# Kernel tuning notes

Measured on AMD Instinct MI355X. Metric: run time of the kernel, lower is better.

The kernel has to match this reference:

```python
import jax, jax.numpy as jnp
import numpy as np

B, S, D, H = 4, 2048, 1024, 16
HD = D // H  # head_dim = 64


def setup_inputs() -> dict:
    key = jax.random.key(0)
    ks = jax.random.split(key, 6)
    scale = 0.02
    x = jax.random.normal(ks[0], (B, S, D), dtype=jnp.float32)
    # per-head projection weights, torch Linear is y = x @ W.T; store as [H, D, HD]
    Wq = jax.random.normal(ks[1], (H, D, HD), dtype=jnp.float32) * scale
    Wk = jax.random.normal(ks[2], (H, D, HD), dtype=jnp.float32) * scale
    Wv = jax.random.normal(ks[3], (H, D, HD), dtype=jnp.float32) * scale
    Wo = jax.random.normal(ks[4], (D, D), dtype=jnp.float32) * scale  # torch [out, in]
    bo = jax.random.normal(ks[5], (D,), dtype=jnp.float32) * scale
    return {"x": x, "Wq": Wq, "Wk": Wk, "Wv": Wv, "Wo": Wo, "bo": bo}


def reference(x, Wq, Wk, Wv, Wo, bo):
    # project: [B,S,D] x [H,D,HD] -> [B,H,S,HD]
    q = jnp.einsum("bsd,hde->bhse", x, Wq)
    k = jnp.einsum("bsd,hde->bhse", x, Wk)
    v = jnp.einsum("bsd,hde->bhse", x, Wv)
    scores = jnp.einsum("bhse,bhte->bhst", q, k) / jnp.sqrt(jnp.float32(HD))
    causal = jnp.tril(jnp.ones((S, S), dtype=bool))  # same as registered tril mask
    scores = jnp.where(causal, scores, -jnp.inf)
    w = jax.nn.softmax(scores, axis=-1)
    out = jnp.einsum("bhst,bhte->bhse", w, v)  # [B,H,S,HD]
    # concat heads along feature dim: [B,S,H*HD] = [B,S,D]
    out = out.transpose(0, 2, 1, 3).reshape(B, S, D)
    # output projection: torch Linear y = x @ W.T + b
    return jnp.einsum("bsd,od->bso", out, Wo) + bo
```

## Files before the change

kernel.cpp:

```cpp
#include <hip/hip_runtime.h>
#include <hip/hip_bf16.h>

typedef __bf16 bf16x8 __attribute__((ext_vector_type(8)));
typedef float f32x4 __attribute__((ext_vector_type(4)));
typedef unsigned short u16x4 __attribute__((ext_vector_type(4)));
typedef unsigned short u16x8 __attribute__((ext_vector_type(8)));
typedef unsigned uint4v __attribute__((ext_vector_type(4)));

#define B_ 4
#define S_ 2048
#define D_ 1024
#define H_ 16
#define HD_ 64

__device__ __forceinline__ unsigned short f2bf(float f) {
  unsigned u = __float_as_uint(f);
  u += 0x7fff + ((u >> 16) & 1);
  return (unsigned short)(u >> 16);
}

__device__ __forceinline__ void gload16(const void* g, void* l) {
  __builtin_amdgcn_global_load_lds((const __attribute__((address_space(1))) unsigned int*)g,
                                   (__attribute__((address_space(3))) unsigned int*)l,
                                   16, 0, 0);
}

__global__ void pack_x_k(const float* __restrict__ in, unsigned short* __restrict__ out, int n4) {
  int i = blockIdx.x * blockDim.x + threadIdx.x;
  int stride = gridDim.x * blockDim.x;
  for (; i < n4; i += stride) {
    float4 v = reinterpret_cast<const float4*>(in)[i];
    u16x4 o = {f2bf(v.x), f2bf(v.y), f2bf(v.z), f2bf(v.w)};
    reinterpret_cast<u16x4*>(out)[i] = o;
  }
}

__global__ void pack_wqkv_k(const float* __restrict__ Wq, const float* __restrict__ Wk,
                            const float* __restrict__ Wv, unsigned short* __restrict__ Wt) {
  int o = blockIdx.x * blockDim.x + threadIdx.x;
  int n = o >> 10;
  int d = o & 1023;
  const float* W = (n < 1024) ? Wq : (n < 2048) ? Wk : Wv;
  int nn = n & 1023;
  int h = nn >> 6, e = nn & 63;
  Wt[o] = f2bf(W[(h << 16) + (d << 6) + e]);
}

__global__ __launch_bounds__(512, 2) void gemm256_k(const unsigned short* __restrict__ A,
                                                    const unsigned short* __restrict__ Bt,
                                                    unsigned short* __restrict__ C,
                                                    int M, int N, int K) {
  __shared__ __align__(16) unsigned short lds[2][2][2][128 * 64];
  const int tid = threadIdx.x;
  const int wid = tid >> 6, lane = tid & 63;
  const int r = lane & 15, g = lane >> 4;
  const int wm = wid >> 2, wn = wid & 3;

  int id = blockIdx.y * gridDim.x + blockIdx.x;
  const int cpx = (gridDim.x * gridDim.y) >> 3;
  id = (id & 7) * cpx + (id >> 3);
  const long arow0 = (long)(id % gridDim.x) * 256;
  const long bcol0 = (long)(id / gridDim.x) * 256;

  const f32x4 z4 = {0.f, 0.f, 0.f, 0.f};
  f32x4 acc[8][4];
#pragma unroll
  for (int m = 0; m < 8; ++m)
#pragma unroll
    for (int n = 0; n < 4; ++n) acc[m][n] = z4;

  auto stage_half = [&](int kt, int op, int h) {
    const unsigned short* src = op ? Bt + (bcol0 + 128 * h) * K : A + (arow0 + 128 * h) * K;
    const int k0 = kt << 6;
    unsigned short* base = &lds[kt & 1][op][h][0];
#pragma unroll
    for (int c = 0; c < 2; ++c) {
      const int j = c * 512 + (wid << 6) + lane;
      const int row = j >> 3, cc = j & 7;
      const int ccs = cc ^ (row & 7);
      gload16(src + (long)row * K + k0 + ccs * 8, base + (c * 512 + (wid << 6)) * 8);
    }
  };

  const int nk = K >> 6;
  stage_half(0, 0, 0);
  stage_half(0, 1, 0);
  stage_half(0, 0, 1);
  stage_half(0, 1, 1);
  stage_half(1, 0, 0);
  stage_half(1, 1, 0);
  asm volatile("s_waitcnt vmcnt(8)" ::: "memory");
  asm volatile("s_barrier" ::: "memory");

  for (int t = 0; t < nk; ++t) {
    const int buf = t & 1;
#pragma unroll
    for (int ph = 0; ph < 4; ++ph) {
      const int mh = ph >> 1, nh = ph & 1;
      bf16x8 af[4][2], bfv[2][2];
#pragma unroll
      for (int i = 0; i < 4; ++i)
#pragma unroll
        for (int kk = 0; kk < 2; ++kk) {
          const int rowh = (2 * i + wm) * 16 + r;
          af[i][kk] = *(const bf16x8*)&lds[buf][0][mh][rowh * 64 + (((kk << 2) + g) ^ (rowh & 7)) * 8];
        }
#pragma unroll
      for (int j = 0; j < 2; ++j)
#pragma unroll
        for (int kk = 0; kk < 2; ++kk) {
          const int rowh = (4 * j + wn) * 16 + r;
          bfv[j][kk] = *(const bf16x8*)&lds[buf][1][nh][rowh * 64 + (((kk << 2) + g) ^ (rowh & 7)) * 8];
        }
      if (ph == 0) { if (t + 1 < nk) stage_half(t + 1, 0, 1); }
      if (ph == 1) { if (t + 1 < nk) stage_half(t + 1, 1, 1); }
      if (ph == 2) { if (t + 2 < nk) stage_half(t + 2, 0, 0); }
      if (ph == 3) { if (t + 2 < nk) stage_half(t + 2, 1, 0); }
      asm volatile("s_barrier" ::: "memory");
      __builtin_amdgcn_s_setprio(1);
#pragma unroll
      for (int kk = 0; kk < 2; ++kk)
#pragma unroll
        for (int i = 0; i < 4; ++i)
#pragma unroll
          for (int j = 0; j < 2; ++j)
            acc[4 * mh + i][2 * nh + j] = __builtin_amdgcn_mfma_f32_16x16x32_bf16(
                af[i][kk], bfv[j][kk], acc[4 * mh + i][2 * nh + j], 0, 0, 0);
      __builtin_amdgcn_s_setprio(0);
      if (ph == 0) {
        if (t + 1 < nk) asm volatile("s_waitcnt vmcnt(6)" ::: "memory");
        else            asm volatile("s_waitcnt vmcnt(0)" ::: "memory");
      }
      if (ph == 3) {
        if (t + 2 < nk)      asm volatile("s_waitcnt vmcnt(8)" ::: "memory");
        else if (t + 1 < nk) asm volatile("s_waitcnt vmcnt(4)" ::: "memory");
      }
      asm volatile("s_waitcnt lgkmcnt(0)\n\ts_barrier" ::: "memory");
    }
  }

#pragma unroll
  for (int m = 0; m < 8; ++m)
#pragma unroll
    for (int n = 0; n < 4; ++n)
#pragma unroll
      for (int rr = 0; rr < 4; ++rr) {
        const long row = arow0 + (2 * m + wm) * 16 + g * 4 + rr;
        const long col = bcol0 + (4 * n + wn) * 16 + r;
        C[row * N + col] = f2bf(acc[m][n][rr]);
      }
}

__global__ __launch_bounds__(256, 2) void gemm_bt_k(const unsigned short* __restrict__ A,
                                                    const unsigned short* __restrict__ Bt,
                                                    float* __restrict__ C,
                                                    const float* __restrict__ bias,
                                                    int M, int N, int K) {
  __shared__ __align__(16) unsigned short lA[2][128 * 64];
  __shared__ __align__(16) unsigned short lB[2][128 * 64];
  const int tid = threadIdx.x;
  const int wid = tid >> 6, lane = tid & 63;
  const int r = lane & 15, g = lane >> 4;
  const long arow0 = (long)blockIdx.x * 128;
  const long brow0 = (long)blockIdx.y * 128;
  const int wr = (wid >> 1) * 64, wc = (wid & 1) * 64;

  const f32x4 z4 = {0.f, 0.f, 0.f, 0.f};
  f32x4 acc[4][4];
#pragma unroll
  for (int m = 0; m < 4; ++m)
#pragma unroll
    for (int n = 0; n < 4; ++n) acc[m][n] = z4;

  auto stage = [&](int buf, int k0) {
#pragma unroll
    for (int c = 0; c < 4; ++c) {
      const int j = c * 256 + wid * 64 + lane;
      const int row = j >> 3, col = (j & 7) * 8;
      gload16(A + (arow0 + row) * K + k0 + col, &lA[buf][(c * 256 + wid * 64) * 8]);
      gload16(Bt + (brow0 + row) * K + k0 + col, &lB[buf][(c * 256 + wid * 64) * 8]);
    }
  };

  stage(0, 0);
  __syncthreads();
  const int nk = K >> 6;
  for (int kt = 0; kt < nk; ++kt) {
    const int cur = kt & 1;
    if (kt + 1 < nk) stage(cur ^ 1, (kt + 1) << 6);
#pragma unroll
    for (int kk = 0; kk < 2; ++kk) {
      bf16x8 af[4], bfr[4];
#pragma unroll
      for (int m = 0; m < 4; ++m)
        af[m] = *(const bf16x8*)&lA[cur][(wr + m * 16 + r) * 64 + kk * 32 + g * 8];
#pragma unroll
      for (int n = 0; n < 4; ++n)
        bfr[n] = *(const bf16x8*)&lB[cur][(wc + n * 16 + r) * 64 + kk * 32 + g * 8];
#pragma unroll
      for (int m = 0; m < 4; ++m)
#pragma unroll
        for (int n = 0; n < 4; ++n)
          acc[m][n] = __builtin_amdgcn_mfma_f32_16x16x32_bf16(af[m], bfr[n], acc[m][n], 0, 0, 0);
    }
    __syncthreads();
  }

#pragma unroll
  for (int m = 0; m < 4; ++m) {
#pragma unroll
    for (int n = 0; n < 4; ++n) {
#pragma unroll
      for (int rr = 0; rr < 4; ++rr) {
        const long row = arow0 + wr + m * 16 + g * 4 + rr;
        const long col = brow0 + wc + n * 16 + r;
        C[row * N + col] = acc[m][n][rr] + bias[col];
      }
    }
  }
}

__global__ __launch_bounds__(256, 2) void attn_k(const unsigned short* __restrict__ qkv,
                                                 unsigned short* __restrict__ out) {
  __shared__ __align__(16) unsigned short lK[2][64 * 64];
  __shared__ __align__(16) unsigned short lVt[2][64 * 64];

  const int tid = threadIdx.x, wid = tid >> 6, lane = tid & 63;
  const int r = lane & 15, g = lane >> 4;
  const int bh = blockIdx.x;
  const int b = bh >> 4, h = bh & 15;
  const int qb = 15 - (int)blockIdx.y;
  const int q0 = qb * 128;

  const long base = ((long)b * S_) * 3072 + h * 64;
  const unsigned short* Qg = qkv + base;
  const unsigned short* Kg = qkv + base + 1024;
  const unsigned short* Vg = qkv + base + 2048;

  int qrow[2];
  bf16x8 qf[2][2];
#pragma unroll
  for (int qs = 0; qs < 2; ++qs) {
    qrow[qs] = q0 + qs * 64 + wid * 16 + r;
#pragma unroll
    for (int kk = 0; kk < 2; ++kk)
      qf[qs][kk] = *(const bf16x8*)&Qg[(long)qrow[qs] * 3072 + kk * 32 + g * 8];
  }

  const f32x4 z4 = {0.f, 0.f, 0.f, 0.f};
  f32x4 o[2][4];
#pragma unroll
  for (int qs = 0; qs < 2; ++qs)
#pragma unroll
    for (int nt = 0; nt < 4; ++nt) o[qs][nt] = z4;
  float m_i[2] = {-1e30f, -1e30f};
  float l_i[2] = {0.f, 0.f};

  u16x8 kreg[2], vreg[2];
  auto load_regs = [&](int t0) {
#pragma unroll
    for (int c = 0; c < 2; ++c) {
      const int j = c * 256 + tid;
      const int tt = j >> 3, e0 = (j & 7) * 8;
      kreg[c] = *(const u16x8*)&Kg[(long)(t0 + tt) * 3072 + e0];
      const int tc = j & 63, ec = j >> 6;
      vreg[c] = *(const u16x8*)&Vg[(long)(t0 + tc) * 3072 + ec * 8];
    }
  };
  auto write_lds = [&](int buf) {
#pragma unroll
    for (int c = 0; c < 2; ++c) {
      const int j = c * 256 + tid;
      const int row = j >> 3, cc = j & 7;
      *(u16x8*)&lK[buf][(row * 8 + (cc ^ (row & 7))) * 8] = kreg[c];
      const int tc = j & 63, ec = j >> 6;
#pragma unroll
      for (int i = 0; i < 8; ++i) {
        const int e = ec * 8 + i;
        lVt[buf][e * 64 + (tc ^ (i * 8))] = vreg[c][i];
      }
    }
  };

  const int ntiles = (q0 >> 6) + 2;
  load_regs(0);
  write_lds(0);

  for (int t = 0; t < ntiles; ++t) {
    const int cur = t & 1;
    if (t + 1 < ntiles) load_regs((t + 1) << 6);
    __syncthreads();

    const int t0 = t << 6;
    const bool act0 = (t < ntiles - 1);
    const bool diag0 = (t == ntiles - 2);
    const bool diag1 = (t == ntiles - 1);

    f32x4 st[2][4];
#pragma unroll
    for (int tt = 0; tt < 4; ++tt) { st[0][tt] = z4; st[1][tt] = z4; }
    __builtin_amdgcn_s_setprio(1);
#pragma unroll
    for (int kk = 0; kk < 2; ++kk)
#pragma unroll
      for (int tt = 0; tt < 4; ++tt) {
        const int row = tt * 16 + r, cc = kk * 4 + g;
        bf16x8 kf = *(const bf16x8*)&lK[cur][(row * 8 + (cc ^ (row & 7))) * 8];
        st[1][tt] = __builtin_amdgcn_mfma_f32_16x16x32_bf16(kf, qf[1][kk], st[1][tt], 0, 0, 0);
        if (act0)
          st[0][tt] = __builtin_amdgcn_mfma_f32_16x16x32_bf16(kf, qf[0][kk], st[0][tt], 0, 0, 0);
      }
    __builtin_amdgcn_s_setprio(0);

    bf16x8 pf[2][2];
    unsigned corr_bits[2] = {0x3f800000u, 0x3f800000u};
    bool dodef[2] = {true, true};
#pragma unroll
    for (int qs = 0; qs < 2; ++qs) {
      if (qs == 0 && !act0) continue;
      const bool diag = qs ? diag1 : diag0;
      float sv[16];
#pragma unroll
      for (int tt = 0; tt < 4; ++tt)
#pragma unroll
        for (int rg = 0; rg < 4; ++rg) {
          float s = st[qs][tt][rg] * 0.125f;
          if (diag && (t0 + tt * 16 + g * 4 + rg > qrow[qs])) s = -1e30f;
          sv[tt * 4 + rg] = s;
        }
      float h0 = fmaxf(fmaxf(fmaxf(sv[0], sv[1]), fmaxf(sv[2], sv[3])),
                       fmaxf(fmaxf(sv[4], sv[5]), fmaxf(sv[6], sv[7])));
      float h1 = fmaxf(fmaxf(fmaxf(sv[8], sv[9]), fmaxf(sv[10], sv[11])),
                       fmaxf(fmaxf(sv[12], sv[13]), fmaxf(sv[14], sv[15])));
      const float pmax = fmaxf(h0, h1);
      const bool defer = __all(pmax - m_i[qs] <= 8.f);
      float corr = 1.f;
      if (!defer) {
        float mx = fmaxf(pmax, m_i[qs]);
        mx = fmaxf(mx, __shfl_xor(mx, 16, 64));
        mx = fmaxf(mx, __shfl_xor(mx, 32, 64));
        corr = __expf(m_i[qs] - mx);
        m_i[qs] = mx;
      }
      dodef[qs] = defer;
      corr_bits[qs] = __float_as_uint(corr);
      float p[16];
      float rs = 0.f;
#pragma unroll
      for (int i = 0; i < 16; ++i) {
        p[i] = __expf(sv[i] - m_i[qs]);
        rs += p[i];
      }
      rs += __shfl_xor(rs, 16, 64);
      rs += __shfl_xor(rs, 32, 64);
      l_i[qs] = l_i[qs] * corr + rs;
      unsigned cw[4][2];
#pragma unroll
      for (int tt = 0; tt < 4; ++tt)
#pragma unroll
        for (int e = 0; e < 2; ++e)
          asm("v_cvt_pk_bf16_f32 %0, %1, %2"
              : "=v"(cw[tt][e]) : "v"(p[tt * 4 + 2 * e]), "v"(p[tt * 4 + 2 * e + 1]));
#pragma unroll
      for (int kk = 0; kk < 2; ++kk) {
        unsigned x0 = cw[2 * kk][0], y0 = cw[2 * kk + 1][0];
        unsigned x1 = cw[2 * kk][1], y1 = cw[2 * kk + 1][1];
        asm volatile("v_permlane32_swap_b32 %0, %1" : "+v"(x0), "+v"(y0));
        asm volatile("v_permlane16_swap_b32 %0, %1" : "+v"(x0), "+v"(y0));
        asm volatile("v_permlane32_swap_b32 %0, %1" : "+v"(x1), "+v"(y1));
        asm volatile("v_permlane16_swap_b32 %0, %1" : "+v"(x1), "+v"(y1));
        uint4v w = {x0, x1, y0, y1};
        pf[qs][kk] = *(bf16x8*)&w;
      }
    }
#pragma unroll
    for (int qs = 0; qs < 2; ++qs) {
      if (qs == 0 && !act0) continue;
      if (!dodef[qs]) {
        const float corr = __uint_as_float(corr_bits[qs]);
#pragma unroll
        for (int rr = 0; rr < 4; ++rr) {
          const float c = __shfl(corr, g * 4 + rr, 64);
#pragma unroll
          for (int nt = 0; nt < 4; ++nt) o[qs][nt][rr] *= c;
        }
      }
    }

    __builtin_amdgcn_s_setprio(1);
#pragma unroll
    for (int kk = 0; kk < 2; ++kk)
#pragma unroll
      for (int nt = 0; nt < 4; ++nt) {
        const int row = nt * 16 + r, cc = kk * 4 + g;
        const bf16x8 vf = *(const bf16x8*)&lVt[cur][(row * 8 + (cc ^ (row & 7))) * 8];
        o[1][nt] = __builtin_amdgcn_mfma_f32_16x16x32_bf16(pf[1][kk], vf, o[1][nt], 0, 0, 0);
        if (act0)
          o[0][nt] = __builtin_amdgcn_mfma_f32_16x16x32_bf16(pf[0][kk], vf, o[0][nt], 0, 0, 0);
      }
    __builtin_amdgcn_s_setprio(0);

    if (t + 1 < ntiles) write_lds(cur ^ 1);
  }

#pragma unroll
  for (int qs = 0; qs < 2; ++qs) {
    float linv[4];
#pragma unroll
    for (int rr = 0; rr < 4; ++rr)
      linv[rr] = 1.f / __shfl(l_i[qs], g * 4 + rr, 64);
#pragma unroll
    for (int nt = 0; nt < 4; ++nt)
#pragma unroll
      for (int rr = 0; rr < 4; ++rr) {
        const long s = q0 + qs * 64 + wid * 16 + g * 4 + rr;
        out[((long)b * S_ + s) * 1024 + h * 64 + nt * 16 + r] = f2bf(o[qs][nt][rr] * linv[rr]);
      }
  }
}

extern "C" void kernel_launch(void* const* d_in, const int* in_sizes, int n_in,
                              void* d_out, int out_size, void* d_ws, size_t ws_size,
                              hipStream_t stream) {
  const float* x = (const float*)d_in[0];
  const float* Wq = (const float*)d_in[1];
  const float* Wk = (const float*)d_in[2];
  const float* Wv = (const float*)d_in[3];
  const float* Wo = (const float*)d_in[4];
  const float* bo = (const float*)d_in[5];
  float* out = (float*)d_out;

  char* ws = (char*)d_ws;
  unsigned short* Xb = (unsigned short*)(ws);
  unsigned short* Wt = (unsigned short*)(ws + (16ul << 20));
  unsigned short* Wob = (unsigned short*)(ws + (22ul << 20));
  unsigned short* QKV = (unsigned short*)(ws + (24ul << 20));
  unsigned short* AO = (unsigned short*)(ws + (72ul << 20));

  pack_x_k<<<2048, 256, 0, stream>>>(x, Xb, (B_ * S_ * D_) / 4);
  pack_x_k<<<512, 256, 0, stream>>>(Wo, Wob, (D_ * D_) / 4);
  pack_wqkv_k<<<(3 * D_ * D_) / 256, 256, 0, stream>>>(Wq, Wk, Wv, Wt);

  gemm256_k<<<dim3(32, 12), 512, 0, stream>>>(Xb, Wt, QKV, B_ * S_, 3 * D_, D_);
  attn_k<<<dim3(64, 16), 256, 0, stream>>>(QKV, AO);
  gemm_bt_k<<<dim3(64, 8), 256, 0, stream>>>(AO, Wob, out, bo, B_ * S_, D_, D_);
}
```

Baseline: 199.3 us.

## Reuse LDS fragments across quadrants and remap blocks to XCDs in QKV GEMM

Restructures the 256x256 GEMM main loop so that A and B fragments read from LDS are kept in registers and reused across the four output quadrants, in a snake order of (0,0),(0,1),(1,1),(1,0). This cuts per-iteration LDS reads from four A plus four B half-reads to two of each. The prefetch depth drops from two k-tiles to one, with vmcnt waits retuned to match. Block-to-tile mapping is also changed to a hardcoded XCD-aware layout (8x6 tiles per XCD group) that assumes a specific grid shape, which trades generality and latency hiding for less LDS traffic and better L2 locality.

```diff
diff --git a/kernel.cpp b/kernel.cpp
--- a/kernel.cpp
+++ b/kernel.cpp
@@ -56,11 +56,10 @@
   const int r = lane & 15, g = lane >> 4;
   const int wm = wid >> 2, wn = wid & 3;
 
-  int id = blockIdx.y * gridDim.x + blockIdx.x;
-  const int cpx = (gridDim.x * gridDim.y) >> 3;
-  id = (id & 7) * cpx + (id >> 3);
-  const long arow0 = (long)(id % gridDim.x) * 256;
-  const long bcol0 = (long)(id / gridDim.x) * 256;
+  const int i_hw = blockIdx.y * gridDim.x + blockIdx.x;
+  const int xcd = i_hw & 7, j = i_hw >> 3;
+  const long arow0 = (long)((xcd & 3) * 8 + (j & 7)) * 256;
+  const long bcol0 = (long)((xcd >> 2) * 6 + (j >> 3)) * 256;
 
   const f32x4 z4 = {0.f, 0.f, 0.f, 0.f};
   f32x4 acc[8][4];
@@ -75,68 +74,80 @@
     unsigned short* base = &lds[kt & 1][op][h][0];
 #pragma unroll
     for (int c = 0; c < 2; ++c) {
-      const int j = c * 512 + (wid << 6) + lane;
-      const int row = j >> 3, cc = j & 7;
+      const int jj = c * 512 + (wid << 6) + lane;
+      const int row = jj >> 3, cc = jj & 7;
       const int ccs = cc ^ (row & 7);
       gload16(src + (long)row * K + k0 + ccs * 8, base + (c * 512 + (wid << 6)) * 8);
     }
+  };
+
+  bf16x8 af[4][2], bv0[2][2], bv1[2][2];
+  auto read_a = [&](int buf, int mh) {
+#pragma unroll
+    for (int i2 = 0; i2 < 4; ++i2)
+#pragma unroll
+      for (int kk = 0; kk < 2; ++kk) {
+        const int rowh = (2 * i2 + wm) * 16 + r;
+        af[i2][kk] = *(const bf16x8*)&lds[buf][0][mh][rowh * 64 + (((kk << 2) + g) ^ (rowh & 7)) * 8];
+      }
+  };
+  auto read_b = [&](bf16x8 (&bv)[2][2], int buf, int nh) {
+#pragma unroll
+    for (int j2 = 0; j2 < 2; ++j2)
+#pragma unroll
+      for (int kk = 0; kk < 2; ++kk) {
+        const int rowh = (4 * j2 + wn) * 16 + r;
+        bv[j2][kk] = *(const bf16x8*)&lds[buf][1][nh][rowh * 64 + (((kk << 2) + g) ^ (rowh & 7)) * 8];
+      }
+  };
+  auto mma_q = [&](bf16x8 (&bv)[2][2], int mh, int nh) {
+    __builtin_amdgcn_s_setprio(1);
+#pragma unroll
+    for (int kk = 0; kk < 2; ++kk)
+#pragma unroll
+      for (int i2 = 0; i2 < 4; ++i2)
+#pragma unroll
+        for (int j2 = 0; j2 < 2; ++j2)
+          acc[4 * mh + i2][2 * nh + j2] = __builtin_amdgcn_mfma_f32_16x16x32_bf16(
+              af[i2][kk], bv[j2][kk], acc[4 * mh + i2][2 * nh + j2], 0, 0, 0);
+    __builtin_amdgcn_s_setprio(0);
   };
 
   const int nk = K >> 6;
   stage_half(0, 0, 0);
   stage_half(0, 1, 0);
+  stage_half(0, 1, 1);
   stage_half(0, 0, 1);
-  stage_half(0, 1, 1);
-  stage_half(1, 0, 0);
-  stage_half(1, 1, 0);
-  asm volatile("s_waitcnt vmcnt(8)" ::: "memory");
+  asm volatile("s_waitcnt vmcnt(4)" ::: "memory");
   asm volatile("s_barrier" ::: "memory");
 
   for (int t = 0; t < nk; ++t) {
     const int buf = t & 1;
-#pragma unroll
-    for (int ph = 0; ph < 4; ++ph) {
-      const int mh = ph >> 1, nh = ph & 1;
-      bf16x8 af[4][2], bfv[2][2];
-#pragma unroll
-      for (int i = 0; i < 4; ++i)
-#pragma unroll
-        for (int kk = 0; kk < 2; ++kk) {
-          const int rowh = (2 * i + wm) * 16 + r;
-          af[i][kk] = *(const bf16x8*)&lds[buf][0][mh][rowh * 64 + (((kk << 2) + g) ^ (rowh & 7)) * 8];
-        }
-#pragma unroll
-      for (int j = 0; j < 2; ++j)
-#pragma unroll
-        for (int kk = 0; kk < 2; ++kk) {
-          const int rowh = (4 * j + wn) * 16 + r;
-          bfv[j][kk] = *(const bf16x8*)&lds[buf][1][nh][rowh * 64 + (((kk << 2) + g) ^ (rowh & 7)) * 8];
-        }
-      if (ph == 0) { if (t + 1 < nk) stage_half(t + 1, 0, 1); }
-      if (ph == 1) { if (t + 1 < nk) stage_half(t + 1, 1, 1); }
-      if (ph == 2) { if (t + 2 < nk) stage_half(t + 2, 0, 0); }
-      if (ph == 3) { if (t + 2 < nk) stage_half(t + 2, 1, 0); }
-      asm volatile("s_barrier" ::: "memory");
-      __builtin_amdgcn_s_setprio(1);
-#pragma unroll
-      for (int kk = 0; kk < 2; ++kk)
-#pragma unroll
-        for (int i = 0; i < 4; ++i)
-#pragma unroll
-          for (int j = 0; j < 2; ++j)
-            acc[4 * mh + i][2 * nh + j] = __builtin_amdgcn_mfma_f32_16x16x32_bf16(
-                af[i][kk], bfv[j][kk], acc[4 * mh + i][2 * nh + j], 0, 0, 0);
-      __builtin_amdgcn_s_setprio(0);
-      if (ph == 0) {
-        if (t + 1 < nk) asm volatile("s_waitcnt vmcnt(6)" ::: "memory");
-        else            asm volatile("s_waitcnt vmcnt(0)" ::: "memory");
-      }
-      if (ph == 3) {
-        if (t + 2 < nk)      asm volatile("s_waitcnt vmcnt(8)" ::: "memory");
-        else if (t + 1 < nk) asm volatile("s_waitcnt vmcnt(4)" ::: "memory");
-      }
-      asm volatile("s_waitcnt lgkmcnt(0)\n\ts_barrier" ::: "memory");
-    }
+    const bool pre = (t + 1 < nk);
+    read_a(buf, 0);
+    read_b(bv0, buf, 0);
+    if (pre) { stage_half(t + 1, 0, 0); stage_half(t + 1, 1, 0); }
+    asm volatile("s_barrier" ::: "memory");
+    mma_q(bv0, 0, 0);
+    if (pre) asm volatile("s_waitcnt vmcnt(6)" ::: "memory");
+    else     asm volatile("s_waitcnt vmcnt(2)" ::: "memory");
+    asm volatile("s_waitcnt lgkmcnt(0)\n\ts_barrier" ::: "memory");
+    read_b(bv1, buf, 1);
+    if (pre) stage_half(t + 1, 1, 1);
+    asm volatile("s_barrier" ::: "memory");
+    mma_q(bv1, 0, 1);
+    if (pre) asm volatile("s_waitcnt vmcnt(6)" ::: "memory");
+    else     asm volatile("s_waitcnt vmcnt(0)" ::: "memory");
+    asm volatile("s_waitcnt lgkmcnt(0)\n\ts_barrier" ::: "memory");
+    read_a(buf, 1);
+    if (pre) stage_half(t + 1, 0, 1);
+    asm volatile("s_barrier" ::: "memory");
+    mma_q(bv1, 1, 1);
+    asm volatile("s_waitcnt lgkmcnt(0)\n\ts_barrier" ::: "memory");
+    asm volatile("s_barrier" ::: "memory");
+    mma_q(bv0, 1, 0);
+    if (pre) asm volatile("s_waitcnt vmcnt(4)" ::: "memory");
+    asm volatile("s_waitcnt lgkmcnt(0)\n\ts_barrier" ::: "memory");
   }
 
 #pragma unroll
```

Result: faster. 188.5 us (-5.4%).
